# Kernel optimization log

Measured on AMD Instinct MI355X. Metric: run time of the kernel, lower is better.

Reference implementation:

```python
import jax, jax.numpy as jnp
import numpy as np

KLD_BINS = 10
RATIO_KLD = 0.5
# categorical one-hot blocks in the 99-dim Adult encoding
BLOCKS = [(1, 8), (8, 24), (24, 31), (31, 45), (45, 51), (51, 53), (53, 55), (58, 99)]
CONT_COLS = np.array([0, 55, 56, 57])


def _cross_entropy(logits, onehot):
    # F.cross_entropy with targets = argmax of the one-hot block (mean over batch)
    logp = jax.nn.log_softmax(logits, axis=-1)
    return -jnp.mean(jnp.sum(onehot * logp, axis=-1))


def _kl_divergence(p, q):
    # np-style KL: sum p*log(p/q) over valid (nonzero) bins
    valid = (p > 0) & (q > 0)
    ratio = jnp.where(valid, p / jnp.where(valid, q, 1.0), 1.0)
    return jnp.sum(jnp.where(valid, p * jnp.log(ratio), 0.0))


def setup_inputs() -> dict:
    B = 262144
    key = jax.random.key(0)
    ks = jax.random.split(key, 16)
    data_decoded = jax.random.normal(ks[0], (B, 99), dtype=jnp.float32)
    # data_true: continuous columns + one-hot categorical blocks
    data_true = jnp.zeros((B, 99), dtype=jnp.float32)
    data_true = data_true.at[:, CONT_COLS].set(jax.random.normal(ks[1], (B, 4), dtype=jnp.float32))
    for j, (s, e) in enumerate(BLOCKS):
        lab = jax.random.randint(ks[2 + j], (B,), 0, e - s)
        data_true = data_true.at[:, s:e].set(jax.nn.one_hot(lab, e - s, dtype=jnp.float32))
    data_encoded = jax.random.normal(ks[11], (B, 12), dtype=jnp.float32)
    sex = jax.random.bernoulli(ks[12], 0.5, (B,)).astype(jnp.float32)
    data_encoded = data_encoded.at[:, 11].set(sex)  # column 11 of combined is the 0/1 sex neuron
    label_true = jax.random.normal(ks[13], (B, 2), dtype=jnp.float32)
    return {
        'data_encoded': data_encoded,
        'data_decoded': data_decoded,
        'data_true': data_true,
        'label_true': label_true,
        'batch_size': B,
    }


def reference(data_encoded, data_decoded, data_true, label_true, batch_size):
    # --- reconstruction MSE on continuous columns ---
    cc = jnp.asarray(CONT_COLS)
    mse_loss = jnp.sum(jnp.mean((data_decoded[:, cc] - data_true[:, cc]) ** 2, axis=0))
    # --- cross-entropy on each categorical block ---
    ce_loss = jnp.float32(0.0)
    for s, e in BLOCKS:
        ce_loss = ce_loss + _cross_entropy(data_decoded[:, s:e], data_true[:, s:e])
    # --- per-feature histogram KLD between male/female groups (no grad, as in torch via .numpy()) ---
    comb = jnp.concatenate([data_encoded, label_true], axis=1)  # [B, 14]
    feats = comb[:, :KLD_BINS]  # first 10 encoded features, [B, 10]
    mn = jnp.min(feats, axis=0)  # per-column min over full batch (torch .item())
    mx = jnp.max(feats, axis=0)
    width = jnp.maximum(mx - mn, 1e-12)
    # torch.histc bin index: floor((x-min)/(max-min)*bins), x==max -> last bin
    idx = jnp.clip(jnp.floor((feats - mn) / width * KLD_BINS).astype(jnp.int32), 0, KLD_BINS - 1)
    onehot = jax.nn.one_hot(idx, KLD_BINS, dtype=jnp.float32)  # [B, 10, bins]
    sexcol = comb[:, 11]
    m_mask = (sexcol == 0).astype(jnp.float32)
    f_mask = (sexcol == 1).astype(jnp.float32)
    m_count = jnp.maximum(jnp.sum(m_mask), 1.0)
    f_count = jnp.maximum(jnp.sum(f_mask), 1.0)
    m_hist = jnp.einsum('b,bik->ik', m_mask, onehot) / m_count  # [10, bins]
    f_hist = jnp.einsum('b,bik->ik', f_mask, onehot) / f_count
    kld = jax.lax.stop_gradient(_kl_divergence(m_hist, f_hist))
    alpha = RATIO_KLD
    multi_loss = (1.0 - alpha) * (mse_loss + ce_loss) + alpha * kld
    return (multi_loss, mse_loss, ce_loss, alpha * kld)
```

## Files before the change

kernel.cpp:

```cpp
#include <hip/hip_runtime.h>
#include <math.h>

#define B_ROWS 262144

#define WS_A 0
#define WS_B 2816
#define WS_C 28416

__device__ __forceinline__ unsigned int map_f(float x) {
  unsigned int b = __float_as_uint(x);
  return (b & 0x80000000u) ? ~b : (b | 0x80000000u);
}
__device__ __forceinline__ float unmap_f(unsigned int u) {
  unsigned int b = (u & 0x80000000u) ? (u ^ 0x80000000u) : ~u;
  return __uint_as_float(b);
}

__global__ __launch_bounds__(256) void k_minmax(const float* __restrict__ enc,
                                                unsigned int* __restrict__ ws) {
  int tid = threadIdx.x, bid = blockIdx.x;
  const float4* e4 = (const float4*)enc;
  float mn[10], mx[10];
  #pragma unroll
  for (int j = 0; j < 10; j++) { mn[j] = 1e30f; mx[j] = -1e30f; }
  unsigned int cm = 0, cf = 0;
  #pragma unroll
  for (int i = 0; i < 8; i++) {
    size_t g = (size_t)bid * 2048 + i * 256 + tid;
    float4 a = e4[g * 3 + 0], b = e4[g * 3 + 1], c = e4[g * 3 + 2];
    float v[12] = {a.x,a.y,a.z,a.w,b.x,b.y,b.z,b.w,c.x,c.y,c.z,c.w};
    #pragma unroll
    for (int j = 0; j < 10; j++) { mn[j] = fminf(mn[j], v[j]); mx[j] = fmaxf(mx[j], v[j]); }
    cm += (v[11] == 0.0f); cf += (v[11] == 1.0f);
  }
  #pragma unroll
  for (int off = 32; off; off >>= 1) {
    #pragma unroll
    for (int j = 0; j < 10; j++) {
      mn[j] = fminf(mn[j], __shfl_xor(mn[j], off));
      mx[j] = fmaxf(mx[j], __shfl_xor(mx[j], off));
    }
    cm += __shfl_xor(cm, off); cf += __shfl_xor(cf, off);
  }
  __shared__ float smn[4][10], smx[4][10];
  __shared__ unsigned int sc[4][2];
  int wave = tid >> 6, lane = tid & 63;
  if (lane == 0) {
    #pragma unroll
    for (int j = 0; j < 10; j++) { smn[wave][j] = mn[j]; smx[wave][j] = mx[j]; }
    sc[wave][0] = cm; sc[wave][1] = cf;
  }
  __syncthreads();
  unsigned int* out = ws + WS_A + bid * 22;
  if (tid < 10) {
    float m = fminf(fminf(smn[0][tid], smn[1][tid]), fminf(smn[2][tid], smn[3][tid]));
    out[tid] = map_f(m);
  } else if (tid < 20) {
    int j = tid - 10;
    float m = fmaxf(fmaxf(smx[0][j], smx[1][j]), fmaxf(smx[2][j], smx[3][j]));
    out[tid] = map_f(m);
  } else if (tid < 22) {
    int j = tid - 20;
    out[tid] = sc[0][j] + sc[1][j] + sc[2][j] + sc[3][j];
  }
}

__global__ __launch_bounds__(256) void k_hist(const float* __restrict__ enc,
                                              unsigned int* __restrict__ ws) {
  __shared__ float mnv[10], wid[10];
  __shared__ unsigned int h[200];
  int tid = threadIdx.x, bid = blockIdx.x;
  for (int i = tid; i < 200; i += 256) h[i] = 0u;
  if (tid < 10) {
    unsigned int umn = 0xFFFFFFFFu, umx = 0u;
    #pragma unroll 4
    for (int b = 0; b < 128; b++) {
      umn = min(umn, ws[WS_A + b * 22 + tid]);
      umx = max(umx, ws[WS_A + b * 22 + 10 + tid]);
    }
    float mn = unmap_f(umn);
    mnv[tid] = mn;
    wid[tid] = fmaxf(unmap_f(umx) - mn, 1e-12f);
  }
  __syncthreads();
  const float4* e4 = (const float4*)enc;
  #pragma unroll
  for (int i = 0; i < 8; i++) {
    size_t g = (size_t)bid * 2048 + i * 256 + tid;
    float4 a = e4[g * 3 + 0], b = e4[g * 3 + 1], c = e4[g * 3 + 2];
    float v[12] = {a.x,a.y,a.z,a.w,b.x,b.y,b.z,b.w,c.x,c.y,c.z,c.w};
    int base = (v[11] == 0.0f) ? 0 : ((v[11] == 1.0f) ? 100 : -1);
    if (base >= 0) {
      #pragma unroll
      for (int cc = 0; cc < 10; cc++) {
        float t = (v[cc] - mnv[cc]) / wid[cc] * 10.0f;
        int bi = min(max((int)floorf(t), 0), 9);
        atomicAdd(&h[base + cc * 10 + bi], 1u);
      }
    }
  }
  __syncthreads();
  if (tid < 200) ws[WS_B + bid * 200 + tid] = h[tid];
}

__global__ __launch_bounds__(256) void k_main(const float* __restrict__ d,
                                              const float* __restrict__ t,
                                              unsigned int* __restrict__ ws) {
  __shared__ float tile[128 * 101];
  __shared__ float red[12];
  int tid = threadIdx.x, bid = blockIdx.x;
  float mse = 0.f, dot = 0.f, ce = 0.f;

  #pragma unroll
  for (int it = 0; it < 2; it++) {
    int tileIdx = bid + it * 1024;
    const float4* d4 = (const float4*)(d + (size_t)tileIdx * 12672);
    const float4* t4 = (const float4*)(t + (size_t)tileIdx * 12672);
    for (int f = tid; f < 3168; f += 256) {
      float4 xd = d4[f];
      float4 xt = t4[f];
      int e = f * 4;
      int r = e / 99;
      int c = e - r * 99;
      float dv[4] = {xd.x, xd.y, xd.z, xd.w};
      float tv[4] = {xt.x, xt.y, xt.z, xt.w};
      #pragma unroll
      for (int k = 0; k < 4; k++) {
        int cc = c + k, rr = r;
        if (cc >= 99) { cc -= 99; rr++; }
        bool cont = (cc == 0) | ((unsigned)(cc - 55) <= 2u);
        float diff = dv[k] - tv[k];
        if (cont) mse += diff * diff;
        else      dot += tv[k] * dv[k];
        tile[rr * 101 + cc] = dv[k];
      }
    }
    __syncthreads();
    if (tid < 128) {
      const float* row = &tile[tid * 101];
      float Z;
      Z = 0.f;
      #pragma unroll
      for (int c = 1; c < 8; c++) Z += __expf(row[c]);
      ce += __logf(Z);
      Z = 0.f;
      #pragma unroll
      for (int c = 8; c < 24; c++) Z += __expf(row[c]);
      ce += __logf(Z);
      Z = 0.f;
      #pragma unroll
      for (int c = 24; c < 31; c++) Z += __expf(row[c]);
      ce += __logf(Z);
      Z = 0.f;
      #pragma unroll
      for (int c = 31; c < 45; c++) Z += __expf(row[c]);
      ce += __logf(Z);
      Z = 0.f;
      #pragma unroll
      for (int c = 45; c < 51; c++) Z += __expf(row[c]);
      ce += __logf(Z);
    } else {
      const float* row = &tile[(tid - 128) * 101];
      float Z;
      Z = 0.f;
      #pragma unroll
      for (int c = 51; c < 53; c++) Z += __expf(row[c]);
      ce += __logf(Z);
      Z = 0.f;
      #pragma unroll
      for (int c = 53; c < 55; c++) Z += __expf(row[c]);
      ce += __logf(Z);
      Z = 0.f;
      #pragma unroll
      for (int c = 58; c < 99; c++) Z += __expf(row[c]);
      ce += __logf(Z);
    }
    __syncthreads();
  }

  #pragma unroll
  for (int off = 32; off; off >>= 1) {
    mse += __shfl_xor(mse, off);
    dot += __shfl_xor(dot, off);
    ce  += __shfl_xor(ce,  off);
  }
  int wave = tid >> 6, lane = tid & 63;
  if (lane == 0) { red[wave] = mse; red[4 + wave] = dot; red[8 + wave] = ce; }
  __syncthreads();
  if (tid == 0) {
    float* C = (float*)(ws + WS_C);
    C[bid]        = red[0] + red[1] + red[2]  + red[3];
    C[1024 + bid] = red[4] + red[5] + red[6]  + red[7];
    C[2048 + bid] = red[8] + red[9] + red[10] + red[11];
  }
}

__global__ __launch_bounds__(256) void k_final(const unsigned int* __restrict__ ws,
                                               float* __restrict__ out) {
  __shared__ float h[200];
  __shared__ float part[256];
  __shared__ float red3[12];
  __shared__ float cnts[2];
  int tid = threadIdx.x;
  if (tid < 200) {
    unsigned int s = 0;
    #pragma unroll 4
    for (int b = 0; b < 128; b++) s += ws[WS_B + b * 200 + tid];
    h[tid] = (float)s;
  }
  if (tid == 200 || tid == 201) {
    unsigned int s = 0;
    #pragma unroll 4
    for (int b = 0; b < 128; b++) s += ws[WS_A + b * 22 + 20 + (tid - 200)];
    cnts[tid - 200] = fmaxf((float)s, 1.0f);
  }
  const float* C = (const float*)(ws + WS_C);
  float msum = 0.f, dsum = 0.f, csum = 0.f;
  for (int i = tid; i < 1024; i += 256) {
    msum += C[i]; dsum += C[1024 + i]; csum += C[2048 + i];
  }
  #pragma unroll
  for (int off = 32; off; off >>= 1) {
    msum += __shfl_xor(msum, off);
    dsum += __shfl_xor(dsum, off);
    csum += __shfl_xor(csum, off);
  }
  int wave = tid >> 6, lane = tid & 63;
  if (lane == 0) { red3[wave] = msum; red3[4 + wave] = dsum; red3[8 + wave] = csum; }
  __syncthreads();
  float term = 0.f;
  if (tid < 100) {
    float mc = h[tid], fc = h[100 + tid];
    if (mc > 0.f && fc > 0.f) {
      float p = mc / cnts[0];
      float q = fc / cnts[1];
      term = p * logf(p / q);
    }
  }
  part[tid] = term;
  __syncthreads();
  for (int s = 128; s; s >>= 1) {
    if (tid < s) part[tid] += part[tid + s];
    __syncthreads();
  }
  if (tid == 0) {
    const float invB = 1.0f / (float)B_ROWS;
    float mse = (red3[0] + red3[1] + red3[2] + red3[3]) * invB;
    float dd  = (red3[4] + red3[5] + red3[6] + red3[7]);
    float cc  = (red3[8] + red3[9] + red3[10] + red3[11]);
    float ce  = (cc - dd) * invB;
    float akld = 0.5f * part[0];
    out[0] = 0.5f * (mse + ce) + akld;
    out[1] = mse;
    out[2] = ce;
    out[3] = akld;
  }
}

extern "C" void kernel_launch(void* const* d_in, const int* in_sizes, int n_in,
                              void* d_out, int out_size, void* d_ws, size_t ws_size,
                              hipStream_t stream) {
  const float* enc = (const float*)d_in[0];
  const float* dec = (const float*)d_in[1];
  const float* tru = (const float*)d_in[2];
  unsigned int* ws = (unsigned int*)d_ws;
  float* out = (float*)d_out;

  hipLaunchKernelGGL(k_minmax, dim3(128),  dim3(256), 0, stream, enc, ws);
  hipLaunchKernelGGL(k_hist,   dim3(128),  dim3(256), 0, stream, enc, ws);
  hipLaunchKernelGGL(k_main,   dim3(1024), dim3(256), 0, stream, dec, tru, ws);
  hipLaunchKernelGGL(k_final,  dim3(1),    dim3(256), 0, stream, ws, out);
}
```

Measured before the change: 274.7 us.

## Restructure main loss kernel into single-wave blocks with 64-row tiles

```diff
diff --git a/kernel.cpp b/kernel.cpp
--- a/kernel.cpp
+++ b/kernel.cpp
@@ -6,6 +6,8 @@
 #define WS_A 0
 #define WS_B 2816
 #define WS_C 28416
+#define MAIN_BLOCKS 2048
+#define N_TILES 4096
 
 __device__ __forceinline__ unsigned int map_f(float x) {
   unsigned int b = __float_as_uint(x);
@@ -103,78 +105,71 @@
   if (tid < 200) ws[WS_B + bid * 200 + tid] = h[tid];
 }
 
-__global__ __launch_bounds__(256) void k_main(const float* __restrict__ d,
-                                              const float* __restrict__ t,
-                                              unsigned int* __restrict__ ws) {
-  __shared__ float tile[128 * 101];
-  __shared__ float red[12];
-  int tid = threadIdx.x, bid = blockIdx.x;
+__global__ __launch_bounds__(64, 2) void k_main(const float* __restrict__ d,
+                                                const float* __restrict__ t,
+                                                unsigned int* __restrict__ ws) {
+  __shared__ float lds[6336];
+  int lane = threadIdx.x, bid = blockIdx.x;
   float mse = 0.f, dot = 0.f, ce = 0.f;
 
-  #pragma unroll
-  for (int it = 0; it < 2; it++) {
-    int tileIdx = bid + it * 1024;
-    const float4* d4 = (const float4*)(d + (size_t)tileIdx * 12672);
-    const float4* t4 = (const float4*)(t + (size_t)tileIdx * 12672);
-    for (int f = tid; f < 3168; f += 256) {
+  for (int tileIdx = bid; tileIdx < N_TILES; tileIdx += MAIN_BLOCKS) {
+    const float4* d4 = (const float4*)d + (size_t)tileIdx * 1584;
+    const float4* t4 = (const float4*)t + (size_t)tileIdx * 1584;
+    float4* l4 = (float4*)lds;
+    #pragma unroll 5
+    for (int f = lane; f < 1584; f += 64) {
       float4 xd = d4[f];
       float4 xt = t4[f];
+      l4[f] = xd;
       int e = f * 4;
-      int r = e / 99;
-      int c = e - r * 99;
+      int c = e - (e / 99) * 99;
       float dv[4] = {xd.x, xd.y, xd.z, xd.w};
       float tv[4] = {xt.x, xt.y, xt.z, xt.w};
       #pragma unroll
       for (int k = 0; k < 4; k++) {
-        int cc = c + k, rr = r;
-        if (cc >= 99) { cc -= 99; rr++; }
+        int cc = c + k;
+        if (cc >= 99) cc -= 99;
         bool cont = (cc == 0) | ((unsigned)(cc - 55) <= 2u);
         float diff = dv[k] - tv[k];
         if (cont) mse += diff * diff;
         else      dot += tv[k] * dv[k];
-        tile[rr * 101 + cc] = dv[k];
       }
     }
     __syncthreads();
-    if (tid < 128) {
-      const float* row = &tile[tid * 101];
-      float Z;
-      Z = 0.f;
-      #pragma unroll
-      for (int c = 1; c < 8; c++) Z += __expf(row[c]);
-      ce += __logf(Z);
-      Z = 0.f;
-      #pragma unroll
-      for (int c = 8; c < 24; c++) Z += __expf(row[c]);
-      ce += __logf(Z);
-      Z = 0.f;
-      #pragma unroll
-      for (int c = 24; c < 31; c++) Z += __expf(row[c]);
-      ce += __logf(Z);
-      Z = 0.f;
-      #pragma unroll
-      for (int c = 31; c < 45; c++) Z += __expf(row[c]);
-      ce += __logf(Z);
-      Z = 0.f;
-      #pragma unroll
-      for (int c = 45; c < 51; c++) Z += __expf(row[c]);
-      ce += __logf(Z);
-    } else {
-      const float* row = &tile[(tid - 128) * 101];
-      float Z;
-      Z = 0.f;
-      #pragma unroll
-      for (int c = 51; c < 53; c++) Z += __expf(row[c]);
-      ce += __logf(Z);
-      Z = 0.f;
-      #pragma unroll
-      for (int c = 53; c < 55; c++) Z += __expf(row[c]);
-      ce += __logf(Z);
-      Z = 0.f;
-      #pragma unroll
-      for (int c = 58; c < 99; c++) Z += __expf(row[c]);
-      ce += __logf(Z);
-    }
+    const float* row = lds + lane * 99;
+    float Z;
+    Z = 0.f;
+    #pragma unroll
+    for (int c = 1; c < 8; c++) Z += __expf(row[c]);
+    ce += __logf(Z);
+    Z = 0.f;
+    #pragma unroll
+    for (int c = 8; c < 24; c++) Z += __expf(row[c]);
+    ce += __logf(Z);
+    Z = 0.f;
+    #pragma unroll
+    for (int c = 24; c < 31; c++) Z += __expf(row[c]);
+    ce += __logf(Z);
+    Z = 0.f;
+    #pragma unroll
+    for (int c = 31; c < 45; c++) Z += __expf(row[c]);
+    ce += __logf(Z);
+    Z = 0.f;
+    #pragma unroll
+    for (int c = 45; c < 51; c++) Z += __expf(row[c]);
+    ce += __logf(Z);
+    Z = 0.f;
+    #pragma unroll
+    for (int c = 51; c < 53; c++) Z += __expf(row[c]);
+    ce += __logf(Z);
+    Z = 0.f;
+    #pragma unroll
+    for (int c = 53; c < 55; c++) Z += __expf(row[c]);
+    ce += __logf(Z);
+    Z = 0.f;
+    #pragma unroll
+    for (int c = 58; c < 99; c++) Z += __expf(row[c]);
+    ce += __logf(Z);
     __syncthreads();
   }
 
@@ -184,14 +179,11 @@
     dot += __shfl_xor(dot, off);
     ce  += __shfl_xor(ce,  off);
   }
-  int wave = tid >> 6, lane = tid & 63;
-  if (lane == 0) { red[wave] = mse; red[4 + wave] = dot; red[8 + wave] = ce; }
-  __syncthreads();
-  if (tid == 0) {
+  if (lane == 0) {
     float* C = (float*)(ws + WS_C);
-    C[bid]        = red[0] + red[1] + red[2]  + red[3];
-    C[1024 + bid] = red[4] + red[5] + red[6]  + red[7];
-    C[2048 + bid] = red[8] + red[9] + red[10] + red[11];
+    C[bid]                   = mse;
+    C[MAIN_BLOCKS + bid]     = dot;
+    C[2 * MAIN_BLOCKS + bid] = ce;
   }
 }
 
@@ -216,8 +208,8 @@
   }
   const float* C = (const float*)(ws + WS_C);
   float msum = 0.f, dsum = 0.f, csum = 0.f;
-  for (int i = tid; i < 1024; i += 256) {
-    msum += C[i]; dsum += C[1024 + i]; csum += C[2048 + i];
+  for (int i = tid; i < MAIN_BLOCKS; i += 256) {
+    msum += C[i]; dsum += C[MAIN_BLOCKS + i]; csum += C[2 * MAIN_BLOCKS + i];
   }
   #pragma unroll
   for (int off = 32; off; off >>= 1) {
@@ -266,8 +258,8 @@
   unsigned int* ws = (unsigned int*)d_ws;
   float* out = (float*)d_out;
 
-  hipLaunchKernelGGL(k_minmax, dim3(128),  dim3(256), 0, stream, enc, ws);
-  hipLaunchKernelGGL(k_hist,   dim3(128),  dim3(256), 0, stream, enc, ws);
-  hipLaunchKernelGGL(k_main,   dim3(1024), dim3(256), 0, stream, dec, tru, ws);
-  hipLaunchKernelGGL(k_final,  dim3(1),    dim3(256), 0, stream, ws, out);
-}
+  hipLaunchKernelGGL(k_minmax, dim3(128),         dim3(256), 0, stream, enc, ws);
+  hipLaunchKernelGGL(k_hist,   dim3(128),         dim3(256), 0, stream, enc, ws);
+  hipLaunchKernelGGL(k_main,   dim3(MAIN_BLOCKS), dim3(64),  0, stream, dec, tru, ws);
+  hipLaunchKernelGGL(k_final,  dim3(1),           dim3(256), 0, stream, ws, out);
+}
```

After: 302.8 us. 1.1x slower.
